# Performance work log

Hardware: AMD Instinct MI355X
Metric: run time of the kernel (lower is better)

Reference implementation:

```python
import jax, jax.numpy as jnp
import numpy as np

B, M, N_, H, C, D = 2, 64, 64, 2, 8, 4  # batch, lattice m, lattice n, heads, channels, head_dim


def get_irpe(R):
    # R: (h, m, n) -> P[h, i, j] = R[h, (xi-xj) mod m, (yi-yj) mod n]
    # (negative fancy-index wrap in the original == modular indexing)
    h, m, n = R.shape
    dx = (jnp.arange(m)[:, None] - jnp.arange(m)[None, :]) % m  # (m, m)
    dy = (jnp.arange(n)[:, None] - jnp.arange(n)[None, :]) % n  # (n, n)
    P = R[:, dx[:, None, :, None], dy[None, :, None, :]]  # (h, m, n, m, n)
    return P.reshape(h, m * n, m * n)


def circ_conv(x, W, b, groups=1):
    # NHWC conv with CIRCULAR padding (flax 'CIRCULAR' == wrap-pad then VALID)
    ph, pw = W.shape[0] // 2, W.shape[1] // 2
    if ph or pw:
        x = jnp.pad(x, ((0, 0), (ph, ph), (pw, pw), (0, 0)), mode='wrap')
    y = jax.lax.conv_general_dilated(x, W, (1, 1), 'VALID',
                                     dimension_numbers=('NHWC', 'HWIO', 'NHWC'),
                                     feature_group_count=groups)
    return y + b


def setup_inputs() -> dict:
    key = jax.random.key(0)
    ks = jax.random.split(key, 10)
    m, n, c, h, d = M, N_, C, H, D

    def nrm(k, shape, fan_in):
        return jax.random.normal(k, shape, jnp.float32) * np.float32(np.sqrt(1.0 / fan_in))

    return {
        'x': jax.random.normal(ks[0], (B, m, n, c), jnp.float32),
        'conv_W': nrm(ks[1], (3, 3, c, c), 9 * c / 2),         # he_normal
        'conv_b': jnp.zeros((c,), jnp.float32),
        'Wq': nrm(ks[2], (c, h * d), c),                       # lecun_normal
        'Wk': nrm(ks[3], (c, h * d), c),
        'Wv': nrm(ks[4], (c, h * d), c),
        'pos': nrm(ks[5], (h, m, n), h * m),                   # lecun_normal on (h,m,n)
        'Wo': nrm(ks[6], (h * d, c), h * d),
        'mlp1_W': nrm(ks[7], (1, 1, c, 4 * c), c / 2),         # he_normal
        'mlp1_b': jnp.zeros((4 * c,), jnp.float32),
        'mlp2_W': nrm(ks[8], (3, 3, 1, 4 * c), 9),             # depthwise, lecun
        'mlp2_b': jnp.zeros((4 * c,), jnp.float32),
        'mlp3_W': nrm(ks[9], (1, 1, 4 * c, c), 4 * c / 2),     # he_normal
        'mlp3_b': jnp.zeros((c,), jnp.float32),
    }


def reference(x, conv_W, conv_b, Wq, Wk, Wv, pos, Wo,
              mlp1_W, mlp1_b, mlp2_W, mlp2_b, mlp3_W, mlp3_b):
    b_, m, n, c = x.shape
    h, d = H, D
    # ---- conv block (norm = 1) ----
    res = x
    x = circ_conv(jax.nn.gelu(x / np.float32(1.0)), conv_W, conv_b) + res
    # ---- attention (norm = 2) ----
    res = x
    y = x / np.float32(np.sqrt(2.0))

    def heads(z, W):
        # (b,m,n,c) @ (c,h*d) -> (b,h,N,d), last dim split order (h,d) as in einops
        return jnp.einsum('bmnc,ce->bmne', z, W).reshape(b_, m * n, h, d).transpose(0, 2, 1, 3)

    q, k, v = heads(y, Wq), heads(y, Wk), heads(y, Wv)
    P = get_irpe(pos)[None]  # (1, h, N, N)
    attn = jax.nn.softmax((jnp.einsum('bhnd,bhmd->bhnm', q, k) + P) / np.float32(np.sqrt(d)))
    # faithful to source: 'bhnn,bhnd->bhnd' uses the DIAGONAL of attn to scale v
    a = jnp.einsum('bhnn,bhnd->bhnd', attn, v)
    a = a.transpose(0, 2, 1, 3).reshape(b_, m * n, h * d)  # b n (h d)
    x = (a @ Wo).reshape(b_, m, n, c) + res
    # ---- MLP (norm = 3) ----
    res = x
    y = x / np.float32(np.sqrt(3.0))
    y = jax.nn.gelu(circ_conv(y, mlp1_W, mlp1_b))
    y = jax.nn.gelu(circ_conv(y, mlp2_W, mlp2_b, groups=4 * c))
    return circ_conv(y, mlp3_W, mlp3_b) + res
```

## Files before the change

kernel.cpp:

```cpp
#include <hip/hip_runtime.h>
#include <math.h>

#define Tt 4096
#define KCH 16

#define QSCALE 0.72134752044448170f

__device__ __forceinline__ float gelu_tanh(float x) {
  float x3 = x * x * x;
  float u2 = 2.3022081159f * (x + 0.044715f * x3);
  float e = __builtin_amdgcn_exp2f(u2);
  float th = 1.0f - 2.0f * __builtin_amdgcn_rcpf(e + 1.0f);
  return 0.5f * x * (1.0f + th);
}

__global__ __launch_bounds__(64) void k_pre(
    const float* __restrict__ x, const float* __restrict__ cW,
    const float* __restrict__ cb, const float* __restrict__ Wq,
    const float* __restrict__ Wk, const float* __restrict__ Wv,
    float* __restrict__ x1, float* __restrict__ qo,
    float* __restrict__ ko, float* __restrict__ vo) {
  const int bi = blockIdx.x;
  const int b = bi >> 6, i = bi & 63;
  const int j = threadIdx.x;
  float acc[8];
#pragma unroll
  for (int c = 0; c < 8; c++) acc[c] = cb[c];
#pragma unroll
  for (int di = 0; di < 3; di++) {
    const int ii = (i + di + 63) & 63;
#pragma unroll
    for (int dj = 0; dj < 3; dj++) {
      const int jj = (j + dj + 63) & 63;
      const float4* px = (const float4*)(x + ((b * 64 + ii) * 64 + jj) * 8);
      float4 a0 = px[0], a1 = px[1];
      float g[8];
      g[0] = gelu_tanh(a0.x); g[1] = gelu_tanh(a0.y);
      g[2] = gelu_tanh(a0.z); g[3] = gelu_tanh(a0.w);
      g[4] = gelu_tanh(a1.x); g[5] = gelu_tanh(a1.y);
      g[6] = gelu_tanh(a1.z); g[7] = gelu_tanh(a1.w);
      const float* w = cW + (di * 3 + dj) * 64;
#pragma unroll
      for (int ci = 0; ci < 8; ci++) {
        const float gv = g[ci];
#pragma unroll
        for (int c = 0; c < 8; c++) acc[c] += gv * w[ci * 8 + c];
      }
    }
  }
  const int t = i * 64 + j;
  const float4* pxc = (const float4*)(x + (b * Tt + t) * 8);
  float4 c0 = pxc[0], c1 = pxc[1];
  float xv[8];
  xv[0] = acc[0] + c0.x; xv[1] = acc[1] + c0.y;
  xv[2] = acc[2] + c0.z; xv[3] = acc[3] + c0.w;
  xv[4] = acc[4] + c1.x; xv[5] = acc[5] + c1.y;
  xv[6] = acc[6] + c1.z; xv[7] = acc[7] + c1.w;
  float4* px1 = (float4*)(x1 + (b * Tt + t) * 8);
  px1[0] = make_float4(xv[0], xv[1], xv[2], xv[3]);
  px1[1] = make_float4(xv[4], xv[5], xv[6], xv[7]);
  float y[8];
#pragma unroll
  for (int c = 0; c < 8; c++) y[c] = xv[c] * 0.7071067811865475f;
#pragma unroll
  for (int h = 0; h < 2; h++) {
    float qe[4], ke[4], ve[4];
#pragma unroll
    for (int d = 0; d < 4; d++) {
      const int e = h * 4 + d;
      float sq = 0.f, sk = 0.f, sv = 0.f;
#pragma unroll
      for (int c = 0; c < 8; c++) {
        sq += y[c] * Wq[c * 8 + e];
        sk += y[c] * Wk[c * 8 + e];
        sv += y[c] * Wv[c * 8 + e];
      }
      qe[d] = sq * QSCALE;
      ke[d] = sk; ve[d] = sv;
    }
    const int idx = (b * 2 + h) * Tt + t;
    ((float4*)qo)[idx] = make_float4(qe[0], qe[1], qe[2], qe[3]);
    ((float4*)ko)[idx] = make_float4(ke[0], ke[1], ke[2], ke[3]);
    ((float4*)vo)[idx] = make_float4(ve[0], ve[1], ve[2], ve[3]);
  }
}

__global__ __launch_bounds__(64) void k_attn(
    const float* __restrict__ qo, const float* __restrict__ ko,
    const float* __restrict__ pos, float* __restrict__ part) {
  const int id = blockIdx.x;
  const int qblk = id & 63;
  const int bh = (id >> 6) & 3;
  const int chunk = id >> 8;
  const int h = bh & 1;
  const int lane = threadIdx.x;
  __shared__ float posr[4][128];
#pragma unroll
  for (int r = 0; r < 4; r++) {
    const int j1 = chunk * 4 + r;
    const int row = (qblk - j1) & 63;
    const float v = QSCALE * pos[(h * 64 + row) * 64 + lane];
    posr[r][lane] = v;
    posr[r][lane + 64] = v;
  }
  __syncthreads();
  const int t1 = qblk * 64 + lane;
  const float4 qv = ((const float4*)qo)[bh * Tt + t1];
  const float4* kp = (const float4*)ko + bh * Tt + chunk * 256;
  float Z0 = 0.0f, Z1 = 0.0f;
#pragma unroll
  for (int r = 0; r < 4; r++) {
    const float* prow = &posr[r][lane + 1];
    const float4* kr = kp + r * 64;
#pragma unroll 8
    for (int j2 = 0; j2 < 64; j2 += 2) {
      const float4 ka = kr[j2];
      const float4 kb = kr[j2 + 1];
      const float ba = prow[63 - j2];
      const float bb = prow[62 - j2];
      const float sa = fmaf(qv.x, ka.x, fmaf(qv.y, ka.y,
                       fmaf(qv.z, ka.z, fmaf(qv.w, ka.w, ba))));
      const float sb = fmaf(qv.x, kb.x, fmaf(qv.y, kb.y,
                       fmaf(qv.z, kb.z, fmaf(qv.w, kb.w, bb))));
      Z0 += __builtin_amdgcn_exp2f(sa);
      Z1 += __builtin_amdgcn_exp2f(sb);
    }
  }
  part[(chunk * 4 + bh) * Tt + t1] = Z0 + Z1;
}

__global__ __launch_bounds__(64) void k_post(
    const float* __restrict__ part, const float* __restrict__ qo,
    const float* __restrict__ ko, const float* __restrict__ vo,
    const float* __restrict__ pos, const float* __restrict__ Wo,
    const float* __restrict__ x1, const float* __restrict__ W1,
    const float* __restrict__ b1, float* __restrict__ x2,
    float* __restrict__ y1) {
  const int gid = blockIdx.x * 64 + threadIdx.x;
  const int b = gid >> 12, t = gid & 4095;
  float a[8];
#pragma unroll
  for (int h = 0; h < 2; h++) {
    const int bh = b * 2 + h;
    float Z = 0.0f;
#pragma unroll
    for (int c = 0; c < KCH; c++) Z += part[(c * 4 + bh) * Tt + t];
    const float4 qv = ((const float4*)qo)[bh * Tt + t];
    const float4 kv = ((const float4*)ko)[bh * Tt + t];
    const float4 vv = ((const float4*)vo)[bh * Tt + t];
    const float s = fmaf(qv.x, kv.x, fmaf(qv.y, kv.y,
                    fmaf(qv.z, kv.z, fmaf(qv.w, kv.w, QSCALE * pos[h * 4096]))));
    const float w = __builtin_amdgcn_exp2f(s) * __builtin_amdgcn_rcpf(Z);
    a[h * 4 + 0] = w * vv.x; a[h * 4 + 1] = w * vv.y;
    a[h * 4 + 2] = w * vv.z; a[h * 4 + 3] = w * vv.w;
  }
  const float4* px1 = (const float4*)(x1 + gid * 8);
  const float4 r0 = px1[0], r1 = px1[1];
  float res[8] = {r0.x, r0.y, r0.z, r0.w, r1.x, r1.y, r1.z, r1.w};
  float xv[8];
#pragma unroll
  for (int c = 0; c < 8; c++) {
    float s = res[c];
#pragma unroll
    for (int e = 0; e < 8; e++) s += a[e] * Wo[e * 8 + c];
    xv[c] = s;
  }
  float4* px2 = (float4*)(x2 + gid * 8);
  px2[0] = make_float4(xv[0], xv[1], xv[2], xv[3]);
  px2[1] = make_float4(xv[4], xv[5], xv[6], xv[7]);
  float y[8];
#pragma unroll
  for (int c = 0; c < 8; c++) y[c] = xv[c] * 0.5773502691896258f;
  float yv[32];
#pragma unroll
  for (int cc = 0; cc < 32; cc++) {
    float s = b1[cc];
#pragma unroll
    for (int c = 0; c < 8; c++) s += y[c] * W1[c * 32 + cc];
    yv[cc] = gelu_tanh(s);
  }
  float4* py = (float4*)(y1 + gid * 32);
#pragma unroll
  for (int qd = 0; qd < 8; qd++)
    py[qd] = make_float4(yv[qd * 4], yv[qd * 4 + 1], yv[qd * 4 + 2], yv[qd * 4 + 3]);
}

__global__ __launch_bounds__(64) void k_mlp23(
    const float* __restrict__ y1, const float* __restrict__ W2,
    const float* __restrict__ b2, const float* __restrict__ W3,
    const float* __restrict__ b3, const float* __restrict__ x2,
    float* __restrict__ out) {
  const int gid = blockIdx.x * 64 + threadIdx.x;
  const int b = gid >> 12, t = gid & 4095;
  const int i = t >> 6, j = t & 63;
  float acc[32];
#pragma unroll
  for (int cc = 0; cc < 32; cc++) acc[cc] = b2[cc];
#pragma unroll
  for (int di = 0; di < 3; di++) {
    const int ii = (i + di + 63) & 63;
#pragma unroll
    for (int dj = 0; dj < 3; dj++) {
      const int jj = (j + dj + 63) & 63;
      const float4* p = (const float4*)(y1 + ((b * 4096 + ii * 64 + jj) * 32));
      const float* w = W2 + (di * 3 + dj) * 32;
#pragma unroll
      for (int cq = 0; cq < 8; cq++) {
        const float4 u = p[cq];
        acc[cq * 4 + 0] += u.x * w[cq * 4 + 0];
        acc[cq * 4 + 1] += u.y * w[cq * 4 + 1];
        acc[cq * 4 + 2] += u.z * w[cq * 4 + 2];
        acc[cq * 4 + 3] += u.w * w[cq * 4 + 3];
      }
    }
  }
#pragma unroll
  for (int cc = 0; cc < 32; cc++) acc[cc] = gelu_tanh(acc[cc]);
  const float4* px2 = (const float4*)(x2 + gid * 8);
  const float4 r0 = px2[0], r1 = px2[1];
  float o[8] = {r0.x + b3[0], r0.y + b3[1], r0.z + b3[2], r0.w + b3[3],
                r1.x + b3[4], r1.y + b3[5], r1.z + b3[6], r1.w + b3[7]};
#pragma unroll
  for (int cc = 0; cc < 32; cc++) {
    const float v = acc[cc];
#pragma unroll
    for (int c = 0; c < 8; c++) o[c] += v * W3[cc * 8 + c];
  }
  float4* po = (float4*)(out + gid * 8);
  po[0] = make_float4(o[0], o[1], o[2], o[3]);
  po[1] = make_float4(o[4], o[5], o[6], o[7]);
}

extern "C" void kernel_launch(void* const* d_in, const int* in_sizes, int n_in,
                              void* d_out, int out_size, void* d_ws, size_t ws_size,
                              hipStream_t stream) {
  const float* x  = (const float*)d_in[0];
  const float* cW = (const float*)d_in[1];
  const float* cb = (const float*)d_in[2];
  const float* Wq = (const float*)d_in[3];
  const float* Wk = (const float*)d_in[4];
  const float* Wv = (const float*)d_in[5];
  const float* pos = (const float*)d_in[6];
  const float* Wo = (const float*)d_in[7];
  const float* W1 = (const float*)d_in[8];
  const float* b1 = (const float*)d_in[9];
  const float* W2 = (const float*)d_in[10];
  const float* b2 = (const float*)d_in[11];
  const float* W3 = (const float*)d_in[12];
  const float* b3 = (const float*)d_in[13];

  float* ws   = (float*)d_ws;
  float* x1   = ws;
  float* qo   = ws + 65536;
  float* ko   = ws + 131072;
  float* vo   = ws + 196608;
  float* part = ws + 262144;
  float* x2   = ws + 524288;
  float* y1   = ws + 589824;
  float* out  = (float*)d_out;

  hipLaunchKernelGGL(k_pre,   dim3(128),  dim3(64), 0, stream, x, cW, cb, Wq, Wk, Wv, x1, qo, ko, vo);
  hipLaunchKernelGGL(k_attn,  dim3(4096), dim3(64), 0, stream, qo, ko, pos, part);
  hipLaunchKernelGGL(k_post,  dim3(128),  dim3(64), 0, stream, part, qo, ko, vo, pos, Wo, x1, W1, b1, x2, y1);
  hipLaunchKernelGGL(k_mlp23, dim3(128),  dim3(64), 0, stream, y1, W2, b2, W3, b3, x2, out);
}
```

Baseline: 117.7 us.

## Use packed FP32 FMA with SGPR-resident interleaved K pairs in attention

The projection kernel now also writes K into a second buffer where each pair of adjacent keys is interleaved per component. The attention kernel reads these pairs as 64-bit block-uniform scalar operands and computes two scores per instruction with inline `v_pk_fma_f32`. It broadcasts q into packed registers and loads the bias pair as one vector. The goal is to halve the FMA instruction count and move K loads off the vector path. The cost is an extra global write in the pre kernel and reliance on inline asm that demands K in SGPRs.

Result: slower. 159.4 us (+35.4%).

```diff
diff --git a/kernel.cpp b/kernel.cpp
--- a/kernel.cpp
+++ b/kernel.cpp
@@ -5,6 +5,15 @@
 #define KCH 16
 
 #define QSCALE 0.72134752044448170f
+
+typedef unsigned long long u64;
+typedef float v2f __attribute__((ext_vector_type(2)));
+
+__device__ __forceinline__ v2f pkfma(v2f a2, u64 k2, v2f c) {
+  v2f d;
+  asm("v_pk_fma_f32 %0, %1, %2, %3" : "=v"(d) : "v"(a2), "s"(k2), "v"(c));
+  return d;
+}
 
 __device__ __forceinline__ float gelu_tanh(float x) {
   float x3 = x * x * x;
@@ -19,7 +28,8 @@
     const float* __restrict__ cb, const float* __restrict__ Wq,
     const float* __restrict__ Wk, const float* __restrict__ Wv,
     float* __restrict__ x1, float* __restrict__ qo,
-    float* __restrict__ ko, float* __restrict__ vo) {
+    float* __restrict__ ko, float* __restrict__ vo,
+    float* __restrict__ kpk) {
   const int bi = blockIdx.x;
   const int b = bi >> 6, i = bi & 63;
   const int j = threadIdx.x;
@@ -82,11 +92,13 @@
     ((float4*)qo)[idx] = make_float4(qe[0], qe[1], qe[2], qe[3]);
     ((float4*)ko)[idx] = make_float4(ke[0], ke[1], ke[2], ke[3]);
     ((float4*)vo)[idx] = make_float4(ve[0], ve[1], ve[2], ve[3]);
+    float* kp2 = kpk + (((size_t)(b * 2 + h) * 2048 + (t >> 1)) << 3) + ((t & 1) ? 0 : 1);
+    kp2[0] = ke[0]; kp2[2] = ke[1]; kp2[4] = ke[2]; kp2[6] = ke[3];
   }
 }
 
 __global__ __launch_bounds__(64) void k_attn(
-    const float* __restrict__ qo, const float* __restrict__ ko,
+    const float* __restrict__ qo, const float* __restrict__ kpk,
     const float* __restrict__ pos, float* __restrict__ part) {
   const int id = blockIdx.x;
   const int qblk = id & 63;
@@ -106,24 +118,24 @@
   __syncthreads();
   const int t1 = qblk * 64 + lane;
   const float4 qv = ((const float4*)qo)[bh * Tt + t1];
-  const float4* kp = (const float4*)ko + bh * Tt + chunk * 256;
+  const v2f qx2 = {qv.x, qv.x}, qy2 = {qv.y, qv.y};
+  const v2f qz2 = {qv.z, qv.z}, qw2 = {qv.w, qv.w};
   float Z0 = 0.0f, Z1 = 0.0f;
 #pragma unroll
   for (int r = 0; r < 4; r++) {
     const float* prow = &posr[r][lane + 1];
-    const float4* kr = kp + r * 64;
+    const u64* kq = (const u64*)kpk + ((size_t)(bh * 2048 + chunk * 128 + r * 32) << 2);
 #pragma unroll 8
-    for (int j2 = 0; j2 < 64; j2 += 2) {
-      const float4 ka = kr[j2];
-      const float4 kb = kr[j2 + 1];
-      const float ba = prow[63 - j2];
-      const float bb = prow[62 - j2];
-      const float sa = fmaf(qv.x, ka.x, fmaf(qv.y, ka.y,
-                       fmaf(qv.z, ka.z, fmaf(qv.w, ka.w, ba))));
-      const float sb = fmaf(qv.x, kb.x, fmaf(qv.y, kb.y,
-                       fmaf(qv.z, kb.z, fmaf(qv.w, kb.w, bb))));
-      Z0 += __builtin_amdgcn_exp2f(sa);
-      Z1 += __builtin_amdgcn_exp2f(sb);
+    for (int jp = 0; jp < 32; jp++) {
+      const v2f bp = *(const v2f*)(prow + 62 - 2 * jp);
+      const u64 kx = kq[jp * 4 + 0], ky = kq[jp * 4 + 1];
+      const u64 kz = kq[jp * 4 + 2], kw = kq[jp * 4 + 3];
+      v2f d = pkfma(qw2, kw, bp);
+      d = pkfma(qz2, kz, d);
+      d = pkfma(qy2, ky, d);
+      d = pkfma(qx2, kx, d);
+      Z0 += __builtin_amdgcn_exp2f(d.x);
+      Z1 += __builtin_amdgcn_exp2f(d.y);
     }
   }
   part[(chunk * 4 + bh) * Tt + t1] = Z0 + Z1;
@@ -257,10 +269,11 @@
   float* part = ws + 262144;
   float* x2   = ws + 524288;
   float* y1   = ws + 589824;
+  float* kpk  = ws + 851968;
   float* out  = (float*)d_out;
 
-  hipLaunchKernelGGL(k_pre,   dim3(128),  dim3(64), 0, stream, x, cW, cb, Wq, Wk, Wv, x1, qo, ko, vo);
-  hipLaunchKernelGGL(k_attn,  dim3(4096), dim3(64), 0, stream, qo, ko, pos, part);
+  hipLaunchKernelGGL(k_pre,   dim3(128),  dim3(64), 0, stream, x, cW, cb, Wq, Wk, Wv, x1, qo, ko, vo, kpk);
+  hipLaunchKernelGGL(k_attn,  dim3(4096), dim3(64), 0, stream, qo, kpk, pos, part);
   hipLaunchKernelGGL(k_post,  dim3(128),  dim3(64), 0, stream, part, qo, ko, vo, pos, Wo, x1, W1, b1, x2, y1);
   hipLaunchKernelGGL(k_mlp23, dim3(128),  dim3(64), 0, stream, y1, W2, b2, W3, b3, x2, out);
 }
```
